# Optimization experiments

Hardware: AMD Instinct MI355X
Metric: run time of the kernel (lower is better)

## Reference

```python
import jax, jax.numpy as jnp
import numpy as np

NZ, N_GEN = 128, 10
H1, H2, IMG = 512, 1024, 784
BATCH = 4096


def setup_inputs() -> dict:
    key = jax.random.key(0)
    ks = jax.random.split(key, 5)
    z = jax.random.normal(ks[0], (BATCH, NZ), dtype=jnp.float32)
    g_idx = jax.random.randint(ks[1], (BATCH,), 0, N_GEN)
    # stacked per-generator MLP weights (fan-in scaled init)
    W1 = jax.random.normal(ks[2], (N_GEN, NZ, H1), dtype=jnp.float32) / np.sqrt(NZ)
    b1 = jnp.zeros((N_GEN, H1), dtype=jnp.float32)
    W2 = jax.random.normal(ks[3], (N_GEN, H1, H2), dtype=jnp.float32) / np.sqrt(H1)
    b2 = jnp.zeros((N_GEN, H2), dtype=jnp.float32)
    W3 = jax.random.normal(ks[4], (N_GEN, H2, IMG), dtype=jnp.float32) / np.sqrt(H2)
    b3 = jnp.zeros((N_GEN, IMG), dtype=jnp.float32)
    return {"z": z, "g_idx": g_idx, "W1": W1, "b1": b1, "W2": W2, "b2": b2, "W3": W3, "b3": b3}


def reference(z, g_idx, W1, b1, W2, b2, W3, b3):
    # Run ALL n_gen sub-generators for every sample (as the torch module does),
    # then gather the chosen branch per sample.
    h = jax.nn.relu(jnp.einsum('bz,gzh->bgh', z, W1) + b1)          # [B, G, H1]
    h = jax.nn.relu(jnp.einsum('bgh,ghk->bgk', h, W2) + b2)         # [B, G, H2]
    images = jnp.tanh(jnp.einsum('bgk,gki->bgi', h, W3) + b3)       # [B, G, IMG]
    # images[arange(B), g_idx]
    out = jnp.take_along_axis(images, g_idx[:, None, None], axis=1)[:, 0]  # [B, IMG]
    return out
```

## Files before the change

kernel.cpp:

```cpp
#include <hip/hip_runtime.h>
#include <math.h>

#define NZ    128
#define H1    512
#define H2    1024
#define IMG   784
#define IMGP  896
#define BATCH 4096
#define NGEN  10
#define MPAD  128

typedef _Float16 f16;
typedef __attribute__((ext_vector_type(8))) _Float16 half8;
typedef __attribute__((ext_vector_type(4))) float floatx4;

#define NB1 ((NZ / 32) * (H1 / 32) * NGEN)
#define NB2 ((H1 / 32) * (H2 / 32) * NGEN)
#define NB3 ((H2 / 32) * (IMGP / 32) * NGEN)

__device__ __forceinline__ void cp16(void* l, const void* g) {
    __builtin_amdgcn_global_load_lds((const __attribute__((address_space(1))) void*)g,
                                     (__attribute__((address_space(3))) void*)l, 16, 0, 0);
}

template<int K, int N, int NPAD>
__device__ __forceinline__ void t_tile(int idx, const float* __restrict__ W,
                                       f16* __restrict__ Wt, f16 (*L)[36]) {
    constexpr int KT = K / 32, NT = NPAD / 32;
    const int g  = idx / (KT * NT);
    const int r2 = idx % (KT * NT);
    const int k0 = (r2 % KT) * 32;
    const int n0 = (r2 / KT) * 32;
    const int t = threadIdx.x;
    {
        const int kk = t >> 3;
        const int nq = (t & 7) * 4;
        float4 v = make_float4(0.f, 0.f, 0.f, 0.f);
        if (n0 + nq < N)
            v = *(const float4*)(W + ((size_t)g * K + (k0 + kk)) * N + n0 + nq);
        L[nq + 0][kk] = (f16)v.x;
        L[nq + 1][kk] = (f16)v.y;
        L[nq + 2][kk] = (f16)v.z;
        L[nq + 3][kk] = (f16)v.w;
    }
    __syncthreads();
    {
        const int nn = t >> 3;
        const int kq = (t & 7) * 4;
        *(ushort4*)(Wt + ((size_t)g * NPAD + (n0 + nn)) * K + k0 + kq) =
            *(const ushort4*)&L[nn][kq];
    }
}

__global__ __launch_bounds__(256)
void prep(const float* __restrict__ W1, const float* __restrict__ W2,
          const float* __restrict__ W3, f16* __restrict__ W1t,
          f16* __restrict__ W2t, f16* __restrict__ W3t,
          const int* __restrict__ g_idx, int* __restrict__ seg,
          int* __restrict__ perm) {
    __shared__ f16 L[32][36];
    __shared__ int lc[NGEN];
    __shared__ int lb[NGEN + 1];
    int bid = blockIdx.x;
    if (bid == 0) {
        const int t = threadIdx.x;
        if (t < NGEN) lc[t] = 0;
        __syncthreads();
        int gv[BATCH / 256];
        #pragma unroll
        for (int i = 0; i < BATCH / 256; ++i) {
            gv[i] = g_idx[t + i * 256];
            atomicAdd(&lc[gv[i]], 1);
        }
        __syncthreads();
        if (t == 0) {
            int s = 0;
            for (int g = 0; g < NGEN; ++g) { lb[g] = s; s += lc[g]; }
            lb[NGEN] = s;
        }
        __syncthreads();
        if (t <= NGEN) seg[t] = lb[t];
        if (t < NGEN) lc[t] = lb[t];
        __syncthreads();
        #pragma unroll
        for (int i = 0; i < BATCH / 256; ++i) {
            int p = atomicAdd(&lc[gv[i]], 1);
            perm[p] = t + i * 256;
        }
        return;
    }
    --bid;
    if (bid < NB1) { t_tile<NZ, H1, H1>(bid, W1, W1t, L); return; }
    bid -= NB1;
    if (bid < NB2) { t_tile<H1, H2, H2>(bid, W2, W2t, L); return; }
    bid -= NB2;
    t_tile<H2, IMG, IMGP>(bid, W3, W3t, L);
}

template<int K, int NOUT, int NPADB, int ACT, int SCATTER, int GATHER>
__global__ __launch_bounds__(256)
void gemm(const f16* __restrict__ Ap, const float* __restrict__ Az,
          const f16* __restrict__ Wt, const float* __restrict__ bias,
          f16* __restrict__ Ch, float* __restrict__ Cout,
          const int* __restrict__ seg, const int* __restrict__ perm) {
    const int g  = blockIdx.z;
    const int s0 = seg[g];
    const int ng = seg[g + 1] - s0;
    const int m0 = blockIdx.x * 64;
    if (m0 >= ng) return;
    const int n0 = blockIdx.y * 128;

    __shared__ f16 As[64 * 64];
    __shared__ f16 Bs[128 * 64];

    const int tid = threadIdx.x, lane = tid & 63, w = tid >> 6;

    const f16* gb[4]; f16* lb[4];
    #pragma unroll
    for (int j = 0; j < 4; ++j) {
        const int r   = w * 32 + j * 8 + (lane >> 3);
        const int swz = ((lane & 7) ^ ((r >> 1) & 7)) * 8;
        gb[j] = Wt + ((size_t)g * NPADB + n0 + r) * K + swz;
        lb[j] = Bs + (w * 32 + j * 8) * 64;
    }

    const f16* ga[2]; f16* la[2];
    const float* gz[2]; f16* aw[2];
    #pragma unroll
    for (int j = 0; j < 2; ++j) {
        const int r   = w * 16 + j * 8 + (lane >> 3);
        const int swz = ((lane & 7) ^ ((r >> 1) & 7)) * 8;
        la[j] = As + (w * 16 + j * 8) * 64;
        if constexpr (GATHER != 0) {
            const int pr = min(s0 + m0 + r, BATCH - 1);
            gz[j] = Az + (size_t)perm[pr] * K + (lane & 7) * 8;
            aw[j] = As + (size_t)r * 64 + swz;
        } else {
            ga[j] = Ap + (size_t)(s0 + m0 + r) * K + swz;
        }
    }

    const int wm = (w & 1) * 32, wn = (w >> 1) * 64;
    const int lm = lane & 15, lq = lane >> 4;

    floatx4 acc[2][4] = {};

    #pragma unroll
    for (int kc = 0; kc < K / 64; ++kc) {
        __syncthreads();
        #pragma unroll
        for (int j = 0; j < 4; ++j) { cp16(lb[j], gb[j]); gb[j] += 64; }
        if constexpr (GATHER != 0) {
            #pragma unroll
            for (int j = 0; j < 2; ++j) {
                const float4 v0 = *(const float4*)(gz[j]);
                const float4 v1 = *(const float4*)(gz[j] + 4);
                gz[j] += 64;
                half8 h;
                h[0] = (f16)v0.x; h[1] = (f16)v0.y; h[2] = (f16)v0.z; h[3] = (f16)v0.w;
                h[4] = (f16)v1.x; h[5] = (f16)v1.y; h[6] = (f16)v1.z; h[7] = (f16)v1.w;
                *(half8*)aw[j] = h;
            }
        } else {
            #pragma unroll
            for (int j = 0; j < 2; ++j) { cp16(la[j], ga[j]); ga[j] += 64; }
        }
        __syncthreads();
        #pragma unroll
        for (int ks = 0; ks < 2; ++ks) {
            half8 a[2], b[4];
            #pragma unroll
            for (int mt = 0; mt < 2; ++mt) {
                const int r  = wm + mt * 16 + lm;
                const int pq = (ks * 4 + lq) ^ ((r >> 1) & 7);
                a[mt] = *(const half8*)&As[r * 64 + pq * 8];
            }
            #pragma unroll
            for (int nf = 0; nf < 4; ++nf) {
                const int r  = wn + (nf >> 1) * 32 + 2 * lm + (nf & 1);
                const int pq = (ks * 4 + lq) ^ ((r >> 1) & 7);
                b[nf] = *(const half8*)&Bs[r * 64 + pq * 8];
            }
            #pragma unroll
            for (int mt = 0; mt < 2; ++mt)
                #pragma unroll
                for (int nf = 0; nf < 4; ++nf)
                    acc[mt][nf] = __builtin_amdgcn_mfma_f32_16x16x32_f16(
                        a[mt], b[nf], acc[mt][nf], 0, 0, 0);
        }
    }

    const int c = n0 + wn + 2 * lm;
    const float* bg = bias + (size_t)g * NOUT;
    const bool in0 = (!SCATTER) || (c < NOUT);
    const bool in1 = (!SCATTER) || (c + 32 < NOUT);
    const float b0 = in0 ? bg[c]      : 0.f;
    const float b1 = in0 ? bg[c + 1]  : 0.f;
    const float b2 = in1 ? bg[c + 32] : 0.f;
    const float b3 = in1 ? bg[c + 33] : 0.f;
    #pragma unroll
    for (int mt = 0; mt < 2; ++mt)
        #pragma unroll
        for (int rr = 0; rr < 4; ++rr) {
            const int gr = m0 + wm + mt * 16 + lq * 4 + rr;
            if (gr >= ng) continue;
            float x0 = acc[mt][0][rr] + b0;
            float x1 = acc[mt][1][rr] + b1;
            float x2 = acc[mt][2][rr] + b2;
            float x3 = acc[mt][3][rr] + b3;
            if (ACT == 0) {
                x0 = fmaxf(x0, 0.f); x1 = fmaxf(x1, 0.f);
                x2 = fmaxf(x2, 0.f); x3 = fmaxf(x3, 0.f);
            } else {
                const float e0 = __expf(2.f * x0);
                const float e1 = __expf(2.f * x1);
                const float e2 = __expf(2.f * x2);
                const float e3 = __expf(2.f * x3);
                x0 = 1.f - 2.f / (e0 + 1.f);
                x1 = 1.f - 2.f / (e1 + 1.f);
                x2 = 1.f - 2.f / (e2 + 1.f);
                x3 = 1.f - 2.f / (e3 + 1.f);
            }
            if (SCATTER) {
                const size_t orow = (size_t)perm[s0 + gr];
                if (in0) *(float2*)&Cout[orow * NOUT + c]      = make_float2(x0, x1);
                if (in1) *(float2*)&Cout[orow * NOUT + c + 32] = make_float2(x2, x3);
            } else {
                union { uint u; f16 h[2]; } o0, o1;
                o0.h[0] = (f16)x0; o0.h[1] = (f16)x1;
                o1.h[0] = (f16)x2; o1.h[1] = (f16)x3;
                *(uint*)&Ch[(size_t)(s0 + gr) * NOUT + c]      = o0.u;
                *(uint*)&Ch[(size_t)(s0 + gr) * NOUT + c + 32] = o1.u;
            }
        }
}

extern "C" void kernel_launch(void* const* d_in, const int* in_sizes, int n_in,
                              void* d_out, int out_size, void* d_ws, size_t ws_size,
                              hipStream_t stream) {
    const float* z    = (const float*)d_in[0];
    const int*   gidx = (const int*)  d_in[1];
    const float* W1   = (const float*)d_in[2];
    const float* b1   = (const float*)d_in[3];
    const float* W2   = (const float*)d_in[4];
    const float* b2   = (const float*)d_in[5];
    const float* W3   = (const float*)d_in[6];
    const float* b3   = (const float*)d_in[7];
    float* out = (float*)d_out;

    char* ws = (char*)d_ws;
    size_t off = 0;
    auto alloc = [&](size_t bytes) { size_t o = off; off = (off + bytes + 255) & ~255ULL; return o; };
    int* seg  = (int*)(ws + alloc((size_t)(NGEN + 1) * 4));
    int* perm = (int*)(ws + alloc((size_t)(BATCH + MPAD) * 4));
    f16* h1p = (f16*)(ws + alloc((size_t)(BATCH + MPAD) * H1 * 2));
    f16* h2p = (f16*)(ws + alloc((size_t)(BATCH + MPAD) * H2 * 2));
    f16* W1t = (f16*)(ws + alloc((size_t)NGEN * H1 * NZ * 2));
    f16* W2t = (f16*)(ws + alloc((size_t)NGEN * H2 * H1 * 2));
    f16* W3t = (f16*)(ws + alloc((size_t)NGEN * IMGP * H2 * 2));

    prep<<<dim3(1 + NB1 + NB2 + NB3), dim3(256), 0, stream>>>(
        W1, W2, W3, W1t, W2t, W3t, gidx, seg, perm);

    gemm<NZ, H1, H1, 0, 0, 1><<<dim3(16, H1 / 128, NGEN), dim3(256), 0, stream>>>(
        nullptr, z, W1t, b1, h1p, nullptr, seg, perm);
    gemm<H1, H2, H2, 0, 0, 0><<<dim3(16, H2 / 128, NGEN), dim3(256), 0, stream>>>(
        h1p, nullptr, W2t, b2, h2p, nullptr, seg, perm);
    gemm<H2, IMG, IMGP, 1, 1, 0><<<dim3(16, IMGP / 128, NGEN), dim3(256), 0, stream>>>(
        h2p, nullptr, W3t, b3, nullptr, out, seg, perm);
}
```

Before: 173.5 us.

## Double-buffer GEMM shared tiles and enlarge weight transpose tiles to 64x64

The grouped GEMM kernel now ping-pongs two shared-memory buffers, issuing the next K-chunk's async loads (and register-staged gathered z loads) before computing on the current chunk. This removes one barrier per iteration and overlaps global loads with MFMA work, at the cost of twice the LDS per block, which may reduce occupancy. The weight prep kernel now transposes 64x64 tiles with 16-byte stores instead of 32x32 tiles, cutting the block count and widening the writes.

```diff
diff --git a/kernel.cpp b/kernel.cpp
--- a/kernel.cpp
+++ b/kernel.cpp
@@ -14,9 +14,9 @@
 typedef __attribute__((ext_vector_type(8))) _Float16 half8;
 typedef __attribute__((ext_vector_type(4))) float floatx4;
 
-#define NB1 ((NZ / 32) * (H1 / 32) * NGEN)
-#define NB2 ((H1 / 32) * (H2 / 32) * NGEN)
-#define NB3 ((H2 / 32) * (IMGP / 32) * NGEN)
+#define TB1 ((NZ / 64) * (H1 / 64) * NGEN)
+#define TB2 ((H1 / 64) * (H2 / 64) * NGEN)
+#define TB3 ((H2 / 64) * (IMGP / 64) * NGEN)
 
 __device__ __forceinline__ void cp16(void* l, const void* g) {
     __builtin_amdgcn_global_load_lds((const __attribute__((address_space(1))) void*)g,
@@ -25,30 +25,38 @@
 
 template<int K, int N, int NPAD>
 __device__ __forceinline__ void t_tile(int idx, const float* __restrict__ W,
-                                       f16* __restrict__ Wt, f16 (*L)[36]) {
-    constexpr int KT = K / 32, NT = NPAD / 32;
+                                       f16* __restrict__ Wt, f16 (*L)[72]) {
+    constexpr int KT = K / 64, NT = NPAD / 64;
     const int g  = idx / (KT * NT);
     const int r2 = idx % (KT * NT);
-    const int k0 = (r2 % KT) * 32;
-    const int n0 = (r2 / KT) * 32;
+    const int k0 = (r2 % KT) * 64;
+    const int n0 = (r2 / KT) * 64;
     const int t = threadIdx.x;
     {
-        const int kk = t >> 3;
-        const int nq = (t & 7) * 4;
-        float4 v = make_float4(0.f, 0.f, 0.f, 0.f);
-        if (n0 + nq < N)
-            v = *(const float4*)(W + ((size_t)g * K + (k0 + kk)) * N + n0 + nq);
-        L[nq + 0][kk] = (f16)v.x;
-        L[nq + 1][kk] = (f16)v.y;
-        L[nq + 2][kk] = (f16)v.z;
-        L[nq + 3][kk] = (f16)v.w;
+        const int kk0 = t >> 4;
+        const int nq  = (t & 15) * 4;
+        #pragma unroll
+        for (int it = 0; it < 4; ++it) {
+            const int kk = kk0 + it * 16;
+            float4 v = make_float4(0.f, 0.f, 0.f, 0.f);
+            if (n0 + nq < N)
+                v = *(const float4*)(W + ((size_t)g * K + (k0 + kk)) * N + n0 + nq);
+            L[nq + 0][kk] = (f16)v.x;
+            L[nq + 1][kk] = (f16)v.y;
+            L[nq + 2][kk] = (f16)v.z;
+            L[nq + 3][kk] = (f16)v.w;
+        }
     }
     __syncthreads();
     {
-        const int nn = t >> 3;
-        const int kq = (t & 7) * 4;
-        *(ushort4*)(Wt + ((size_t)g * NPAD + (n0 + nn)) * K + k0 + kq) =
-            *(const ushort4*)&L[nn][kq];
+        const int nn0 = t >> 3;
+        const int kq  = (t & 7) * 8;
+        #pragma unroll
+        for (int it = 0; it < 2; ++it) {
+            const int nn = nn0 + it * 32;
+            *(half8*)(Wt + ((size_t)g * NPAD + (n0 + nn)) * K + k0 + kq) =
+                *(const half8*)&L[nn][kq];
+        }
     }
 }
 
@@ -58,7 +66,7 @@
           f16* __restrict__ W2t, f16* __restrict__ W3t,
           const int* __restrict__ g_idx, int* __restrict__ seg,
           int* __restrict__ perm) {
-    __shared__ f16 L[32][36];
+    __shared__ f16 L[64][72];
     __shared__ int lc[NGEN];
     __shared__ int lb[NGEN + 1];
     int bid = blockIdx.x;
@@ -90,10 +98,10 @@
         return;
     }
     --bid;
-    if (bid < NB1) { t_tile<NZ, H1, H1>(bid, W1, W1t, L); return; }
-    bid -= NB1;
-    if (bid < NB2) { t_tile<H1, H2, H2>(bid, W2, W2t, L); return; }
-    bid -= NB2;
+    if (bid < TB1) { t_tile<NZ, H1, H1>(bid, W1, W1t, L); return; }
+    bid -= TB1;
+    if (bid < TB2) { t_tile<H1, H2, H2>(bid, W2, W2t, L); return; }
+    bid -= TB2;
     t_tile<H2, IMG, IMGP>(bid, W3, W3t, L);
 }
 
@@ -110,62 +118,83 @@
     if (m0 >= ng) return;
     const int n0 = blockIdx.y * 128;
 
-    __shared__ f16 As[64 * 64];
-    __shared__ f16 Bs[128 * 64];
+    __shared__ f16 As[2][64 * 64];
+    __shared__ f16 Bs[2][128 * 64];
 
     const int tid = threadIdx.x, lane = tid & 63, w = tid >> 6;
 
-    const f16* gb[4]; f16* lb[4];
+    const f16* gb[4]; int lbo[4];
     #pragma unroll
     for (int j = 0; j < 4; ++j) {
         const int r   = w * 32 + j * 8 + (lane >> 3);
         const int swz = ((lane & 7) ^ ((r >> 1) & 7)) * 8;
         gb[j] = Wt + ((size_t)g * NPADB + n0 + r) * K + swz;
-        lb[j] = Bs + (w * 32 + j * 8) * 64;
-    }
-
-    const f16* ga[2]; f16* la[2];
-    const float* gz[2]; f16* aw[2];
+        lbo[j] = (w * 32 + j * 8) * 64;
+    }
+
+    const f16* ga[2]; const float* gz[2]; int lao[2]; int awo[2];
     #pragma unroll
     for (int j = 0; j < 2; ++j) {
         const int r   = w * 16 + j * 8 + (lane >> 3);
         const int swz = ((lane & 7) ^ ((r >> 1) & 7)) * 8;
-        la[j] = As + (w * 16 + j * 8) * 64;
+        lao[j] = (w * 16 + j * 8) * 64;
         if constexpr (GATHER != 0) {
             const int pr = min(s0 + m0 + r, BATCH - 1);
             gz[j] = Az + (size_t)perm[pr] * K + (lane & 7) * 8;
-            aw[j] = As + (size_t)r * 64 + swz;
+            awo[j] = r * 64 + swz;
         } else {
             ga[j] = Ap + (size_t)(s0 + m0 + r) * K + swz;
         }
     }
 
+    float4 rz0[2], rz1[2];
+
     const int wm = (w & 1) * 32, wn = (w >> 1) * 64;
     const int lm = lane & 15, lq = lane >> 4;
 
     floatx4 acc[2][4] = {};
-
-    #pragma unroll
-    for (int kc = 0; kc < K / 64; ++kc) {
-        __syncthreads();
-        #pragma unroll
-        for (int j = 0; j < 4; ++j) { cp16(lb[j], gb[j]); gb[j] += 64; }
-        if constexpr (GATHER != 0) {
+    constexpr int NT = K / 64;
+
+    #pragma unroll
+    for (int j = 0; j < 4; ++j) { cp16(&Bs[0][lbo[j]], gb[j]); gb[j] += 64; }
+    if constexpr (GATHER != 0) {
+        #pragma unroll
+        for (int j = 0; j < 2; ++j) {
+            rz0[j] = *(const float4*)(gz[j]);
+            rz1[j] = *(const float4*)(gz[j] + 4);
+            gz[j] += 64;
+            half8 h;
+            h[0] = (f16)rz0[j].x; h[1] = (f16)rz0[j].y;
+            h[2] = (f16)rz0[j].z; h[3] = (f16)rz0[j].w;
+            h[4] = (f16)rz1[j].x; h[5] = (f16)rz1[j].y;
+            h[6] = (f16)rz1[j].z; h[7] = (f16)rz1[j].w;
+            *(half8*)&As[0][awo[j]] = h;
+        }
+    } else {
+        #pragma unroll
+        for (int j = 0; j < 2; ++j) { cp16(&As[0][lao[j]], ga[j]); ga[j] += 64; }
+    }
+    __syncthreads();
+
+    int cur = 0;
+    #pragma unroll
+    for (int kc = 0; kc < NT; ++kc) {
+        const bool more = (kc + 1 < NT);
+        if (more) {
             #pragma unroll
-            for (int j = 0; j < 2; ++j) {
-                const float4 v0 = *(const float4*)(gz[j]);
-                const float4 v1 = *(const float4*)(gz[j] + 4);
-                gz[j] += 64;
-                half8 h;
-                h[0] = (f16)v0.x; h[1] = (f16)v0.y; h[2] = (f16)v0.z; h[3] = (f16)v0.w;
-                h[4] = (f16)v1.x; h[5] = (f16)v1.y; h[6] = (f16)v1.z; h[7] = (f16)v1.w;
-                *(half8*)aw[j] = h;
-            }
-        } else {
-            #pragma unroll
-            for (int j = 0; j < 2; ++j) { cp16(la[j], ga[j]); ga[j] += 64; }
-        }
-        __syncthreads();
+            for (int j = 0; j < 4; ++j) { cp16(&Bs[cur ^ 1][lbo[j]], gb[j]); gb[j] += 64; }
+            if constexpr (GATHER != 0) {
+                #pragma unroll
+                for (int j = 0; j < 2; ++j) {
+                    rz0[j] = *(const float4*)(gz[j]);
+                    rz1[j] = *(const float4*)(gz[j] + 4);
+                    gz[j] += 64;
+                }
+            } else {
+                #pragma unroll
+                for (int j = 0; j < 2; ++j) { cp16(&As[cur ^ 1][lao[j]], ga[j]); ga[j] += 64; }
+            }
+        }
         #pragma unroll
         for (int ks = 0; ks < 2; ++ks) {
             half8 a[2], b[4];
@@ -173,13 +202,13 @@
             for (int mt = 0; mt < 2; ++mt) {
                 const int r  = wm + mt * 16 + lm;
                 const int pq = (ks * 4 + lq) ^ ((r >> 1) & 7);
-                a[mt] = *(const half8*)&As[r * 64 + pq * 8];
+                a[mt] = *(const half8*)&As[cur][r * 64 + pq * 8];
             }
             #pragma unroll
             for (int nf = 0; nf < 4; ++nf) {
                 const int r  = wn + (nf >> 1) * 32 + 2 * lm + (nf & 1);
                 const int pq = (ks * 4 + lq) ^ ((r >> 1) & 7);
-                b[nf] = *(const half8*)&Bs[r * 64 + pq * 8];
+                b[nf] = *(const half8*)&Bs[cur][r * 64 + pq * 8];
             }
             #pragma unroll
             for (int mt = 0; mt < 2; ++mt)
@@ -187,6 +216,21 @@
                 for (int nf = 0; nf < 4; ++nf)
                     acc[mt][nf] = __builtin_amdgcn_mfma_f32_16x16x32_f16(
                         a[mt], b[nf], acc[mt][nf], 0, 0, 0);
+        }
+        if (more) {
+            if constexpr (GATHER != 0) {
+                #pragma unroll
+                for (int j = 0; j < 2; ++j) {
+                    half8 h;
+                    h[0] = (f16)rz0[j].x; h[1] = (f16)rz0[j].y;
+                    h[2] = (f16)rz0[j].z; h[3] = (f16)rz0[j].w;
+                    h[4] = (f16)rz1[j].x; h[5] = (f16)rz1[j].y;
+                    h[6] = (f16)rz1[j].z; h[7] = (f16)rz1[j].w;
+                    *(half8*)&As[cur ^ 1][awo[j]] = h;
+                }
+            }
+            __syncthreads();
+            cur ^= 1;
         }
     }
 
@@ -259,7 +303,7 @@
     f16* W2t = (f16*)(ws + alloc((size_t)NGEN * H2 * H1 * 2));
     f16* W3t = (f16*)(ws + alloc((size_t)NGEN * IMGP * H2 * 2));
 
-    prep<<<dim3(1 + NB1 + NB2 + NB3), dim3(256), 0, stream>>>(
+    prep<<<dim3(1 + TB1 + TB2 + TB3), dim3(256), 0, stream>>>(
         W1, W2, W3, W1t, W2t, W3t, gidx, seg, perm);
 
     gemm<NZ, H1, H1, 0, 0, 1><<<dim3(16, H1 / 128, NGEN), dim3(256), 0, stream>>>(
```

After: 183.7 us. 1.06x slower.
